# Kernel optimization log

Hardware: AMD Instinct MI355X
Metric: run time of the kernel (lower is better)

Reference implementation:

```python
import jax, jax.numpy as jnp
import numpy as np

B, F, N_SP, VIS_DIM, DIM, HEADS = 2, 16, 784, 512, 512, 8


def setup_inputs() -> dict:
    key = jax.random.key(0)
    k0, k1, k2 = jax.random.split(key, 3)
    x = jax.random.normal(k0, (B, F * N_SP, VIS_DIM), dtype=jnp.float32)
    # QKV: nn.Linear(vis_dim, dim*3, bias=False) -> weight [3*dim, vis_dim]
    Wqkv = jax.random.normal(k1, (3 * DIM, VIS_DIM), dtype=jnp.float32) * 0.02
    # proj: nn.Linear(dim, vis_dim) -> weight [vis_dim, dim], bias [vis_dim]
    Wproj = jax.random.normal(k2, (VIS_DIM, DIM), dtype=jnp.float32) * 0.02
    bproj = jnp.zeros((VIS_DIM,), dtype=jnp.float32)
    return {"x": x, "Wqkv": Wqkv, "Wproj": Wproj, "bproj": bproj,
            "spatial": N_SP, "f": F, "n": N_SP}


def reference(x, Wqkv, Wproj, bproj, spatial, f, n):
    # Factorized (divided space-time) SPATIAL attention:
    # einops_from='b (f n) d', einops_to='(b f) n d' -- attention over n within each frame.
    h = HEADS
    b, seq, _ = x.shape  # seq = f * n
    dim = Wqkv.shape[0] // 3
    hd = dim // h
    scale = hd ** -0.5

    qkv = x @ Wqkv.T                             # [b, f*n, 3*dim]
    q, k, v = jnp.split(qkv, 3, axis=-1)
    rs = lambda t: t.reshape(b, f, n, h, hd)     # b (f n) (h d) -> b f n h d
    q = rs(q) * scale
    k = rs(k)
    v = rs(v)

    # scores over spatial tokens within each (batch, frame, head)
    attn = jax.nn.softmax(jnp.einsum('bfihd,bfjhd->bfhij', q, k), axis=-1)
    out = jnp.einsum('bfhij,bfjhd->bfihd', attn, v)   # [b, f, n, h, hd]
    out = out.reshape(b, seq, dim)               # merge heads + restore (f n)
    return out @ Wproj.T + bproj                 # [b, f*n, vis_dim]
```

## Files before the change

kernel.cpp:

```cpp
#include <hip/hip_runtime.h>
#include <hip/hip_bf16.h>
#include <stdint.h>

using bf16 = __hip_bfloat16;
typedef __bf16 bf16x8 __attribute__((ext_vector_type(8)));
typedef float f32x4  __attribute__((ext_vector_type(4)));
typedef float f32x16 __attribute__((ext_vector_type(16)));

#define NB 2
#define NF 16
#define NSP 784
#define SEQ 12544
#define MROWS 25088
#define QSCALE 0.18033688011112042f

__device__ inline void gload16(const void* g, void* l) {
    __builtin_amdgcn_global_load_lds(
        (const __attribute__((address_space(1))) unsigned int*)g,
        (__attribute__((address_space(3))) unsigned int*)l, 16, 0, 0);
}
__device__ inline ushort f2bu(float x) {
    union { bf16 b; ushort u; } c; c.b = __float2bfloat16(x); return c.u;
}

__global__ __launch_bounds__(256)
void cvt_w_kernel(const float* __restrict__ wqkv, const float* __restrict__ wproj,
                  ushort* __restrict__ wqkvb, ushort* __restrict__ wpb) {
    int i = blockIdx.x * 256 + threadIdx.x;
    float4 v;
    ushort4 u;
    if (i < 196608) {
        float s = (i < 65536) ? QSCALE : 1.0f;
        v = ((const float4*)wqkv)[i];
        u.x = f2bu(v.x * s); u.y = f2bu(v.y * s);
        u.z = f2bu(v.z * s); u.w = f2bu(v.w * s);
        ((ushort4*)wqkvb)[i] = u;
    } else {
        int j = i - 196608;
        v = ((const float4*)wproj)[j];
        u.x = f2bu(v.x); u.y = f2bu(v.y); u.z = f2bu(v.z); u.w = f2bu(v.w);
        ((ushort4*)wpb)[j] = u;
    }
}

template<int EPI>
__global__ __launch_bounds__(256)
void gemm_mfma(const float* __restrict__ Af, const ushort* __restrict__ Ab16,
               const ushort* __restrict__ W, const float* __restrict__ bias,
               ushort* __restrict__ outb, float* __restrict__ outf,
               int K, int ldc, int npan)
{
    constexpr int SWZ = 7;
    __shared__ ushort smem[16384];

    const int tid = threadIdx.x;
    const int bid = blockIdx.x;
    const int gsz = 4 * npan;
    const int r   = bid % gsz;
    const int m0 = ((bid / gsz) * 4 + (r & 3)) * 128;
    const int n0 = (r >> 2) * 128;
    const int l  = tid & 63;
    const int wv = tid >> 6;
    const int wm = wv >> 1, wn = wv & 1;
    const int lm = l & 15;
    const int koffb = (l >> 4) * 16;
    const int swz = (lm & SWZ) << 4;

    const int rsub = tid >> 3;
    const int cb0  = (tid & 7) * 16;
    const int wofs = (tid >> 6) * 512;

    const size_t ldb = (size_t)K * 2;
    const char* Wb = (const char*)W + (size_t)n0 * ldb;
    const char* Ab = (EPI == 1) ? (const char*)Ab16 + (size_t)m0 * ldb : nullptr;
    const float* Afp = (EPI == 0) ? Af + (size_t)m0 * K : nullptr;

    float4 ar0[4], ar1[4];
    if (EPI == 0) {
#pragma unroll
        for (int i = 0; i < 4; ++i) {
            int row = i * 32 + rsub;
            const float* src = Afp + (size_t)row * K + (tid & 7) * 8;
            ar0[i] = *(const float4*)src;
            ar1[i] = *(const float4*)(src + 4);
        }
    }

    f32x4 acc[4][4] = {};

    for (int k0 = 0; k0 < K; k0 += 64) {
        if (k0) __syncthreads();
#pragma unroll
        for (int i = 0; i < 4; ++i) {
            int row = i * 32 + rsub;
            int cbs = cb0 ^ ((row & SWZ) << 4);
            size_t roff = (size_t)row * ldb + (size_t)(k0 * 2 + cbs);
            gload16(Wb + roff, smem + 8192 + i * 2048 + wofs);
            if (EPI == 1) gload16(Ab + roff, smem + i * 2048 + wofs);
        }
        if (EPI == 0) {
#pragma unroll
            for (int i = 0; i < 4; ++i) {
                int row = i * 32 + rsub;
                union { ushort us[8]; bf16x8 v; } pk;
                pk.us[0] = f2bu(ar0[i].x); pk.us[1] = f2bu(ar0[i].y);
                pk.us[2] = f2bu(ar0[i].z); pk.us[3] = f2bu(ar0[i].w);
                pk.us[4] = f2bu(ar1[i].x); pk.us[5] = f2bu(ar1[i].y);
                pk.us[6] = f2bu(ar1[i].z); pk.us[7] = f2bu(ar1[i].w);
                int off = row * 64 + ((cb0 ^ ((row & SWZ) << 4)) >> 1);
                *(bf16x8*)&smem[off] = pk.v;
            }
        }
        __syncthreads();
        if (EPI == 0 && k0 + 64 < K) {
#pragma unroll
            for (int i = 0; i < 4; ++i) {
                int row = i * 32 + rsub;
                const float* src = Afp + (size_t)row * K + (k0 + 64) + (tid & 7) * 8;
                ar0[i] = *(const float4*)src;
                ar1[i] = *(const float4*)(src + 4);
            }
        }

#pragma unroll
        for (int ks = 0; ks < 2; ++ks) {
            bf16x8 af[4], wf[4];
            const int cb = ((ks * 64 + koffb) ^ swz) >> 1;
#pragma unroll
            for (int f = 0; f < 4; ++f) {
                int rA = wm * 64 + f * 16 + lm;
                int rW = wn * 64 + f * 16 + lm;
                af[f] = *(const bf16x8*)&smem[rA * 64 + cb];
                wf[f] = *(const bf16x8*)&smem[8192 + rW * 64 + cb];
            }
            __builtin_amdgcn_s_setprio(1);
#pragma unroll
            for (int fm = 0; fm < 4; ++fm)
#pragma unroll
                for (int fn = 0; fn < 4; ++fn)
                    acc[fm][fn] = __builtin_amdgcn_mfma_f32_16x16x32_bf16(
                        wf[fn], af[fm], acc[fm][fn], 0, 0, 0);
            __builtin_amdgcn_s_setprio(0);
        }
    }

    const int ln4 = (l >> 4) * 4;
    if (EPI == 0) {
#pragma unroll
        for (int fm = 0; fm < 4; ++fm) {
            int m = m0 + wm * 64 + fm * 16 + lm;
            ushort* rowp = outb + (size_t)m * ldc + n0 + wn * 64 + ln4;
#pragma unroll
            for (int fn = 0; fn < 4; ++fn) {
                ushort4 u;
                u.x = f2bu(acc[fm][fn][0]); u.y = f2bu(acc[fm][fn][1]);
                u.z = f2bu(acc[fm][fn][2]); u.w = f2bu(acc[fm][fn][3]);
                *(ushort4*)(rowp + fn * 16) = u;
            }
        }
    } else {
#pragma unroll
        for (int fm = 0; fm < 4; ++fm) {
            int m = m0 + wm * 64 + fm * 16 + lm;
            float* rowp = outf + (size_t)m * ldc + n0 + wn * 64 + ln4;
#pragma unroll
            for (int fn = 0; fn < 4; ++fn) {
                float4 b4 = *(const float4*)&bias[n0 + wn * 64 + fn * 16 + ln4];
                float4 o;
                o.x = acc[fm][fn][0] + b4.x; o.y = acc[fm][fn][1] + b4.y;
                o.z = acc[fm][fn][2] + b4.z; o.w = acc[fm][fn][3] + b4.w;
                *(float4*)(rowp + fn * 16) = o;
            }
        }
    }
}

__global__ __launch_bounds__(256)
void vtrans(const ushort* __restrict__ qkv, ushort* __restrict__ vt)
{
    __shared__ __align__(16) ushort T[256][72];
    const int tid = threadIdx.x;
    const int pr  = blockIdx.x;
    const int c   = blockIdx.y;
    const int hh  = pr & 7, bfi = pr >> 3;
    const ushort* vsrc = qkv + (size_t)bfi * NSP * 1536 + 1024 + hh * 64;
    ushort* dst = vt + (size_t)pr * (64 * NSP);
    const int d = tid & 63, q = tid >> 6;

    const int j0 = c * 256;
    const int nj = (NSP - j0) < 256 ? (NSP - j0) : 256;
    if (tid < nj) {
        const ushort* src = vsrc + (size_t)(j0 + tid) * 1536;
#pragma unroll
        for (int u = 0; u < 8; ++u)
            *(uint4*)&T[tid][u * 8] = *(const uint4*)(src + u * 8);
    }
    __syncthreads();
    if (q * 64 < nj) {
        int cnt = nj - q * 64; if (cnt > 64) cnt = 64;
        union { uint4 u[8]; ushort s[64]; } buf;
#pragma unroll
        for (int jj = 0; jj < 64; ++jj)
            buf.s[jj] = T[q * 64 + jj][d];
        ushort* o = dst + (size_t)d * NSP + j0 + q * 64;
        if (cnt == 64) {
#pragma unroll
            for (int u = 0; u < 8; ++u) *(uint4*)(o + u * 8) = buf.u[u];
        } else {
#pragma unroll
            for (int u = 0; u < 2; ++u) *(uint4*)(o + u * 8) = buf.u[u];
        }
    }
}

__global__ __launch_bounds__(256, 3)
void attn_mfma(const ushort* __restrict__ qkv, const ushort* __restrict__ vt,
               ushort* __restrict__ oh)
{
    __shared__ __align__(16) ushort Ks[3][4096];
    __shared__ __align__(16) ushort Vs[3][4096];
    const int tid = threadIdx.x;
    const int l   = tid & 63;
    const int li  = l & 31;
    const int h5  = l >> 5;
    const int w   = tid >> 6;

    const int bid  = blockIdx.x;
    const int xcd  = bid & 7;
    const int slot = bid >> 3;
    const int pr   = (xcd << 5) + slot / 7;
    const int qt   = slot % 7;
    const int hh   = pr & 7;
    const int bfi  = pr >> 3;
    const size_t rowbase = (size_t)bfi * NSP;
    const int iq = qt * 128 + w * 32 + li;
    const bool qvalid = iq < NSP;
    const int iqc = qvalid ? iq : NSP - 1;

    bf16x8 qf[4];
    {
        const ushort* qrow = qkv + (rowbase + iqc) * 1536 + hh * 64 + h5 * 8;
#pragma unroll
        for (int ks = 0; ks < 4; ++ks)
            qf[ks] = *(const bf16x8*)(qrow + ks * 16);
    }

    const char* kb0   = (const char*)(qkv + rowbase * 1536 + 512 + hh * 64);
    const char* vbase = (const char*)(vt + (size_t)pr * (64 * NSP));

    const int srow = tid >> 3;
    const int sg16 = (tid & 7) * 16;
    const int sswz = sg16 ^ ((srow & 7) << 4);

    float l_run = 0.f;
    f32x16 o0 = {}, o1 = {};

    const int rsw   = (li & 7) << 4;
    const int base0 = li * 128;
    const int base1 = (32 + li) * 128;

#pragma unroll
    for (int u = 0; u < 2; ++u) {
#pragma unroll
        for (int i = 0; i < 2; ++i) {
            int row = i * 32 + srow;
            gload16(kb0 + (size_t)(u * 64 + row) * 3072 + sswz, &Ks[u][i * 2048 + tid * 8]);
            gload16(vbase + (size_t)row * 1568 + u * 128 + sswz, &Vs[u][i * 2048 + tid * 8]);
        }
    }
    asm volatile("s_waitcnt vmcnt(4)" ::: "memory");
    __builtin_amdgcn_s_barrier();

    int rd = 0;
    for (int t = 0; t < 13; ++t) {
        int st = rd + 2; if (st >= 3) st -= 3;
        if (t < 11) {
            const int jn = t * 64 + 128;
#pragma unroll
            for (int i = 0; i < 2; ++i) {
                int row = i * 32 + srow;
                int jr = jn + row; if (jr > NSP - 1) jr = NSP - 1;
                gload16(kb0 + (size_t)jr * 3072 + sswz, &Ks[st][i * 2048 + tid * 8]);
                int cb = jn * 2 + sswz;
                if (cb + 16 > NSP * 2) cb = jn * 2;
                gload16(vbase + (size_t)row * 1568 + cb, &Vs[st][i * 2048 + tid * 8]);
            }
        }

        const char* KsC = (const char*)&Ks[rd][0];
        const char* VsC = (const char*)&Vs[rd][0];

        f32x16 s0 = {}, s1 = {};
        __builtin_amdgcn_s_setprio(1);
#pragma unroll
        for (int ks = 0; ks < 4; ++ks) {
            int cb = (ks * 32 + h5 * 16) ^ rsw;
            bf16x8 k0 = *(const bf16x8*)(KsC + base0 + cb);
            bf16x8 k1 = *(const bf16x8*)(KsC + base1 + cb);
            s0 = __builtin_amdgcn_mfma_f32_32x32x16_bf16(k0, qf[ks], s0, 0, 0, 0);
            s1 = __builtin_amdgcn_mfma_f32_32x32x16_bf16(k1, qf[ks], s1, 0, 0, 0);
        }
        __builtin_amdgcn_s_setprio(0);

        if (t == 12) {
#pragma unroll
            for (int r = 0; r < 16; ++r) {
                int jl = (r & 3) + 8 * (r >> 2) + 4 * h5;
                if (768 + jl >= NSP)      s0[r] = -1e30f;
                if (768 + 32 + jl >= NSP) s1[r] = -1e30f;
            }
        }

        float p0[16], p1[16];
        float rs = 0.f;
#pragma unroll
        for (int r = 0; r < 16; ++r) { p0[r] = exp2f(s0[r]); rs += p0[r]; }
#pragma unroll
        for (int r = 0; r < 16; ++r) { p1[r] = exp2f(s1[r]); rs += p1[r]; }
        rs += __shfl_xor(rs, 32);
        l_run += rs;

#pragma unroll
        for (int js = 0; js < 4; ++js) {
            const int rb8 = (js & 1) * 8;
            float e0 = (js < 2) ? p0[rb8 + 0] : p1[rb8 + 0];
            float e1 = (js < 2) ? p0[rb8 + 1] : p1[rb8 + 1];
            float e2 = (js < 2) ? p0[rb8 + 2] : p1[rb8 + 2];
            float e3 = (js < 2) ? p0[rb8 + 3] : p1[rb8 + 3];
            float e4 = (js < 2) ? p0[rb8 + 4] : p1[rb8 + 4];
            float e5 = (js < 2) ? p0[rb8 + 5] : p1[rb8 + 5];
            float e6 = (js < 2) ? p0[rb8 + 6] : p1[rb8 + 6];
            float e7 = (js < 2) ? p0[rb8 + 7] : p1[rb8 + 7];
            uint A0, A1, B0, B1;
            asm("v_cvt_pk_bf16_f32 %0, %1, %2" : "=v"(A0) : "v"(e0), "v"(e1));
            asm("v_cvt_pk_bf16_f32 %0, %1, %2" : "=v"(A1) : "v"(e2), "v"(e3));
            asm("v_cvt_pk_bf16_f32 %0, %1, %2" : "=v"(B0) : "v"(e4), "v"(e5));
            asm("v_cvt_pk_bf16_f32 %0, %1, %2" : "=v"(B1) : "v"(e6), "v"(e7));
            asm volatile("v_permlane32_swap_b32 %0, %1" : "+v"(A0), "+v"(B0));
            asm volatile("v_permlane32_swap_b32 %0, %1" : "+v"(A1), "+v"(B1));
            union { uint u[4]; bf16x8 v; } pf;
            pf.u[0] = A0; pf.u[1] = A1; pf.u[2] = B0; pf.u[3] = B1;

            int cb = (js * 32 + h5 * 16) ^ rsw;
            bf16x8 v0f = *(const bf16x8*)(VsC + base0 + cb);
            bf16x8 v1f = *(const bf16x8*)(VsC + base1 + cb);
            __builtin_amdgcn_s_setprio(1);
            o0 = __builtin_amdgcn_mfma_f32_32x32x16_bf16(v0f, pf.v, o0, 0, 0, 0);
            o1 = __builtin_amdgcn_mfma_f32_32x32x16_bf16(v1f, pf.v, o1, 0, 0, 0);
            __builtin_amdgcn_s_setprio(0);
        }

        if (t < 12) {
            if (t < 11) asm volatile("s_waitcnt vmcnt(4)" ::: "memory");
            else        asm volatile("s_waitcnt vmcnt(0)" ::: "memory");
            __builtin_amdgcn_s_barrier();
        }
        rd = rd + 1; if (rd >= 3) rd = 0;
    }

    if (qvalid) {
        float inv = 1.0f / l_run;
        size_t ro = (rowbase + iq) * 512 + hh * 64;
#pragma unroll
        for (int g = 0; g < 4; ++g) {
            int d = g * 8 + h5 * 4;
            ushort4 uh0, uh1;
#pragma unroll
            for (int m = 0; m < 4; ++m) {
                ((ushort*)&uh0)[m] = f2bu(o0[g * 4 + m] * inv);
                ((ushort*)&uh1)[m] = f2bu(o1[g * 4 + m] * inv);
            }
            *(ushort4*)&oh[ro + d]      = uh0;
            *(ushort4*)&oh[ro + 32 + d] = uh1;
        }
    }
}

extern "C" void kernel_launch(void* const* d_in, const int* in_sizes, int n_in,
                              void* d_out, int out_size, void* d_ws, size_t ws_size,
                              hipStream_t stream) {
    const float* x     = (const float*)d_in[0];
    const float* Wqkv  = (const float*)d_in[1];
    const float* Wproj = (const float*)d_in[2];
    const float* bproj = (const float*)d_in[3];
    float* out = (float*)d_out;

    char* ws = (char*)d_ws;
    ushort* aout  = (ushort*)(ws);
    ushort* qkvb  = (ushort*)(ws + 25690112);
    ushort* wqkvb = (ushort*)(ws + 102760448);
    ushort* wpb   = (ushort*)(ws + 104333312);

    ushort* vtb = (ushort*)d_out;

    dim3 blk(256);
    cvt_w_kernel<<<1024, blk, 0, stream>>>(Wqkv, Wproj, wqkvb, wpb);

    gemm_mfma<0><<<dim3(2352), blk, 0, stream>>>(
        x, nullptr, wqkvb, nullptr, qkvb, nullptr, 512, 1536, 12);

    vtrans<<<dim3(256, 4), blk, 0, stream>>>(qkvb, vtb);

    attn_mfma<<<dim3(1792), blk, 0, stream>>>(qkvb, vtb, aout);

    gemm_mfma<1><<<dim3(784), blk, 0, stream>>>(
        nullptr, aout, wpb, bproj, nullptr, out, 512, 512, 4);
}
```

Baseline: 211.3 us.

## Use 512-thread attention blocks with double-buffered K/V tiles

The attention kernel now runs 8 waves per block, so each K/V tile loaded into shared memory serves 256 query rows instead of 128. The grid drops to 1024 blocks, with 4 query tiles per (batch, frame, head). The triple-buffered pipeline with vmcnt-based waits becomes a double buffer with a full __syncthreads each iteration. Waves whose query rows fall past the 784-token end skip the compute, which leaves some waves idle in the last tile. The change aims to halve K/V load traffic per query, at the cost of a shallower prefetch pipeline and heavier barriers.

```diff
diff --git a/kernel.cpp b/kernel.cpp
--- a/kernel.cpp
+++ b/kernel.cpp
@@ -213,12 +213,12 @@
     }
 }
 
-__global__ __launch_bounds__(256, 3)
+__global__ __launch_bounds__(512, 8)
 void attn_mfma(const ushort* __restrict__ qkv, const ushort* __restrict__ vt,
                ushort* __restrict__ oh)
 {
-    __shared__ __align__(16) ushort Ks[3][4096];
-    __shared__ __align__(16) ushort Vs[3][4096];
+    __shared__ __align__(16) ushort Ks[2][4096];
+    __shared__ __align__(16) ushort Vs[2][4096];
     const int tid = threadIdx.x;
     const int l   = tid & 63;
     const int li  = l & 31;
@@ -228,17 +228,18 @@
     const int bid  = blockIdx.x;
     const int xcd  = bid & 7;
     const int slot = bid >> 3;
-    const int pr   = (xcd << 5) + slot / 7;
-    const int qt   = slot % 7;
+    const int pr   = (xcd << 5) + (slot >> 2);
+    const int qt   = slot & 3;
     const int hh   = pr & 7;
     const int bfi  = pr >> 3;
     const size_t rowbase = (size_t)bfi * NSP;
-    const int iq = qt * 128 + w * 32 + li;
+    const int iq = qt * 256 + w * 32 + li;
     const bool qvalid = iq < NSP;
+    const bool waveActive = (qt * 256 + w * 32) < NSP;
     const int iqc = qvalid ? iq : NSP - 1;
 
     bf16x8 qf[4];
-    {
+    if (waveActive) {
         const ushort* qrow = qkv + (rowbase + iqc) * 1536 + hh * 64 + h5 * 8;
 #pragma unroll
         for (int ks = 0; ks < 4; ++ks)
@@ -259,103 +260,81 @@
     const int base0 = li * 128;
     const int base1 = (32 + li) * 128;
 
-#pragma unroll
-    for (int u = 0; u < 2; ++u) {
-#pragma unroll
-        for (int i = 0; i < 2; ++i) {
-            int row = i * 32 + srow;
-            gload16(kb0 + (size_t)(u * 64 + row) * 3072 + sswz, &Ks[u][i * 2048 + tid * 8]);
-            gload16(vbase + (size_t)row * 1568 + u * 128 + sswz, &Vs[u][i * 2048 + tid * 8]);
-        }
-    }
-    asm volatile("s_waitcnt vmcnt(4)" ::: "memory");
-    __builtin_amdgcn_s_barrier();
-
-    int rd = 0;
+    gload16(kb0 + (size_t)srow * 3072 + sswz, &Ks[0][tid * 8]);
+    gload16(vbase + (size_t)srow * 1568 + sswz, &Vs[0][tid * 8]);
+    __syncthreads();
+
+    int cur = 0;
     for (int t = 0; t < 13; ++t) {
-        int st = rd + 2; if (st >= 3) st -= 3;
-        if (t < 11) {
-            const int jn = t * 64 + 128;
-#pragma unroll
-            for (int i = 0; i < 2; ++i) {
-                int row = i * 32 + srow;
-                int jr = jn + row; if (jr > NSP - 1) jr = NSP - 1;
-                gload16(kb0 + (size_t)jr * 3072 + sswz, &Ks[st][i * 2048 + tid * 8]);
-                int cb = jn * 2 + sswz;
-                if (cb + 16 > NSP * 2) cb = jn * 2;
-                gload16(vbase + (size_t)row * 1568 + cb, &Vs[st][i * 2048 + tid * 8]);
-            }
-        }
-
-        const char* KsC = (const char*)&Ks[rd][0];
-        const char* VsC = (const char*)&Vs[rd][0];
-
-        f32x16 s0 = {}, s1 = {};
-        __builtin_amdgcn_s_setprio(1);
-#pragma unroll
-        for (int ks = 0; ks < 4; ++ks) {
-            int cb = (ks * 32 + h5 * 16) ^ rsw;
-            bf16x8 k0 = *(const bf16x8*)(KsC + base0 + cb);
-            bf16x8 k1 = *(const bf16x8*)(KsC + base1 + cb);
-            s0 = __builtin_amdgcn_mfma_f32_32x32x16_bf16(k0, qf[ks], s0, 0, 0, 0);
-            s1 = __builtin_amdgcn_mfma_f32_32x32x16_bf16(k1, qf[ks], s1, 0, 0, 0);
-        }
-        __builtin_amdgcn_s_setprio(0);
-
-        if (t == 12) {
+        if (t < 12) {
+            const int jn = t * 64 + 64;
+            int jr = jn + srow; if (jr > NSP - 1) jr = NSP - 1;
+            gload16(kb0 + (size_t)jr * 3072 + sswz, &Ks[cur ^ 1][tid * 8]);
+            int cb = jn * 2 + sswz;
+            if (cb + 16 > NSP * 2) cb = jn * 2;
+            gload16(vbase + (size_t)srow * 1568 + cb, &Vs[cur ^ 1][tid * 8]);
+        }
+
+        if (waveActive) {
+            const char* KsC = (const char*)&Ks[cur][0];
+            const char* VsC = (const char*)&Vs[cur][0];
+
+            f32x16 s0 = {}, s1 = {};
+            __builtin_amdgcn_s_setprio(1);
+#pragma unroll
+            for (int ks = 0; ks < 4; ++ks) {
+                int cb = (ks * 32 + h5 * 16) ^ rsw;
+                bf16x8 k0 = *(const bf16x8*)(KsC + base0 + cb);
+                bf16x8 k1 = *(const bf16x8*)(KsC + base1 + cb);
+                s0 = __builtin_amdgcn_mfma_f32_32x32x16_bf16(k0, qf[ks], s0, 0, 0, 0);
+                s1 = __builtin_amdgcn_mfma_f32_32x32x16_bf16(k1, qf[ks], s1, 0, 0, 0);
+            }
+            __builtin_amdgcn_s_setprio(0);
+
+            if (t == 12) {
+#pragma unroll
+                for (int r = 0; r < 16; ++r) {
+                    int jl = (r & 3) + 8 * (r >> 2) + 4 * h5;
+                    if (768 + jl >= NSP)      s0[r] = -1e30f;
+                    if (768 + 32 + jl >= NSP) s1[r] = -1e30f;
+                }
+            }
+
+            float rs = 0.f;
 #pragma unroll
             for (int r = 0; r < 16; ++r) {
-                int jl = (r & 3) + 8 * (r >> 2) + 4 * h5;
-                if (768 + jl >= NSP)      s0[r] = -1e30f;
-                if (768 + 32 + jl >= NSP) s1[r] = -1e30f;
-            }
-        }
-
-        float p0[16], p1[16];
-        float rs = 0.f;
-#pragma unroll
-        for (int r = 0; r < 16; ++r) { p0[r] = exp2f(s0[r]); rs += p0[r]; }
-#pragma unroll
-        for (int r = 0; r < 16; ++r) { p1[r] = exp2f(s1[r]); rs += p1[r]; }
-        rs += __shfl_xor(rs, 32);
-        l_run += rs;
-
-#pragma unroll
-        for (int js = 0; js < 4; ++js) {
-            const int rb8 = (js & 1) * 8;
-            float e0 = (js < 2) ? p0[rb8 + 0] : p1[rb8 + 0];
-            float e1 = (js < 2) ? p0[rb8 + 1] : p1[rb8 + 1];
-            float e2 = (js < 2) ? p0[rb8 + 2] : p1[rb8 + 2];
-            float e3 = (js < 2) ? p0[rb8 + 3] : p1[rb8 + 3];
-            float e4 = (js < 2) ? p0[rb8 + 4] : p1[rb8 + 4];
-            float e5 = (js < 2) ? p0[rb8 + 5] : p1[rb8 + 5];
-            float e6 = (js < 2) ? p0[rb8 + 6] : p1[rb8 + 6];
-            float e7 = (js < 2) ? p0[rb8 + 7] : p1[rb8 + 7];
-            uint A0, A1, B0, B1;
-            asm("v_cvt_pk_bf16_f32 %0, %1, %2" : "=v"(A0) : "v"(e0), "v"(e1));
-            asm("v_cvt_pk_bf16_f32 %0, %1, %2" : "=v"(A1) : "v"(e2), "v"(e3));
-            asm("v_cvt_pk_bf16_f32 %0, %1, %2" : "=v"(B0) : "v"(e4), "v"(e5));
-            asm("v_cvt_pk_bf16_f32 %0, %1, %2" : "=v"(B1) : "v"(e6), "v"(e7));
-            asm volatile("v_permlane32_swap_b32 %0, %1" : "+v"(A0), "+v"(B0));
-            asm volatile("v_permlane32_swap_b32 %0, %1" : "+v"(A1), "+v"(B1));
-            union { uint u[4]; bf16x8 v; } pf;
-            pf.u[0] = A0; pf.u[1] = A1; pf.u[2] = B0; pf.u[3] = B1;
-
-            int cb = (js * 32 + h5 * 16) ^ rsw;
-            bf16x8 v0f = *(const bf16x8*)(VsC + base0 + cb);
-            bf16x8 v1f = *(const bf16x8*)(VsC + base1 + cb);
-            __builtin_amdgcn_s_setprio(1);
-            o0 = __builtin_amdgcn_mfma_f32_32x32x16_bf16(v0f, pf.v, o0, 0, 0, 0);
-            o1 = __builtin_amdgcn_mfma_f32_32x32x16_bf16(v1f, pf.v, o1, 0, 0, 0);
-            __builtin_amdgcn_s_setprio(0);
-        }
-
-        if (t < 12) {
-            if (t < 11) asm volatile("s_waitcnt vmcnt(4)" ::: "memory");
-            else        asm volatile("s_waitcnt vmcnt(0)" ::: "memory");
-            __builtin_amdgcn_s_barrier();
-        }
-        rd = rd + 1; if (rd >= 3) rd = 0;
+                s0[r] = exp2f(s0[r]); rs += s0[r];
+                s1[r] = exp2f(s1[r]); rs += s1[r];
+            }
+            rs += __shfl_xor(rs, 32);
+            l_run += rs;
+
+#pragma unroll
+            for (int js = 0; js < 4; ++js) {
+                const int rb8 = (js & 1) * 8;
+                const f32x16& s = (js < 2) ? s0 : s1;
+                uint A0, A1, B0, B1;
+                asm("v_cvt_pk_bf16_f32 %0, %1, %2" : "=v"(A0) : "v"(s[rb8+0]), "v"(s[rb8+1]));
+                asm("v_cvt_pk_bf16_f32 %0, %1, %2" : "=v"(A1) : "v"(s[rb8+2]), "v"(s[rb8+3]));
+                asm("v_cvt_pk_bf16_f32 %0, %1, %2" : "=v"(B0) : "v"(s[rb8+4]), "v"(s[rb8+5]));
+                asm("v_cvt_pk_bf16_f32 %0, %1, %2" : "=v"(B1) : "v"(s[rb8+6]), "v"(s[rb8+7]));
+                asm volatile("v_permlane32_swap_b32 %0, %1" : "+v"(A0), "+v"(B0));
+                asm volatile("v_permlane32_swap_b32 %0, %1" : "+v"(A1), "+v"(B1));
+                union { uint u[4]; bf16x8 v; } pf;
+                pf.u[0] = A0; pf.u[1] = A1; pf.u[2] = B0; pf.u[3] = B1;
+
+                int cb = (js * 32 + h5 * 16) ^ rsw;
+                bf16x8 v0f = *(const bf16x8*)(VsC + base0 + cb);
+                bf16x8 v1f = *(const bf16x8*)(VsC + base1 + cb);
+                __builtin_amdgcn_s_setprio(1);
+                o0 = __builtin_amdgcn_mfma_f32_32x32x16_bf16(v0f, pf.v, o0, 0, 0, 0);
+                o1 = __builtin_amdgcn_mfma_f32_32x32x16_bf16(v1f, pf.v, o1, 0, 0, 0);
+                __builtin_amdgcn_s_setprio(0);
+            }
+        }
+
+        __syncthreads();
+        cur ^= 1;
     }
 
     if (qvalid) {
@@ -401,7 +380,7 @@
 
     vtrans<<<dim3(256, 4), blk, 0, stream>>>(qkvb, vtb);
 
-    attn_mfma<<<dim3(1792), blk, 0, stream>>>(qkvb, vtb, aout);
+    attn_mfma<<<dim3(1024), dim3(512), 0, stream>>>(qkvb, vtb, aout);
 
     gemm_mfma<1><<<dim3(784), blk, 0, stream>>>(
         nullptr, aout, wpb, bproj, nullptr, out, 512, 512, 4);
```

Result: slower. 548.8 us (+159.8%).
